# Optimization experiments

Measured on AMD Instinct MI355X. Metric: run time of the kernel, lower is better.

The kernel has to match this reference:

```python
import jax, jax.numpy as jnp
import numpy as np


def setup_inputs() -> dict:
    key = jax.random.key(0)
    k1, k2, k3, k4 = jax.random.split(key, 4)
    in_features, out_features = 4096, 11008
    n_tokens = 64
    x = jax.random.normal(k1, (n_tokens, in_features), dtype=jnp.float32)
    # int8-valued weights stored as int32 (values in [-128, 127] range subset)
    weight_int = jax.random.randint(k2, (out_features, in_features), 0, 127, dtype=jnp.int32)
    weight_scale = jnp.float32(0.01)
    weight_zero_point = 3  # scalar int zero point
    bias = jax.random.normal(k3, (out_features,), dtype=jnp.float32) * 0.02
    return {
        "x": x,
        "weight_int": weight_int,
        "weight_scale": weight_scale,
        "weight_zero_point": weight_zero_point,
        "bias": bias,
    }


def reference(x, weight_int, weight_scale, weight_zero_point, bias):
    # Dequantize: W = (W_int - zp) * scale, shape [out, in]
    w = (weight_int.astype(jnp.float32) - jnp.float32(weight_zero_point)) * weight_scale
    # F.linear: y = x @ W^T + b
    out = jnp.einsum("ti,oi->to", x, w)
    return out + bias
```

## Files before the change

### kernel.cpp

```cpp
#include <hip/hip_runtime.h>
#include <hip/hip_bf16.h>

typedef __attribute__((ext_vector_type(8))) short short8;
typedef __attribute__((ext_vector_type(4))) float f32x4;
typedef __attribute__((ext_vector_type(4))) int   int4v;

#define IN_F   4096
#define OUT_F  11008
#define KSPLIT 2
#define KHALF  (IN_F / KSPLIT)
#define BK     64
#define NIT    (KHALF / BK)
#define DEPTH  4

__device__ __forceinline__ short bf16_rne(float f) {
    unsigned u = __builtin_bit_cast(unsigned, f);
    u += 0x7FFFu + ((u >> 16) & 1u);
    return (short)(u >> 16);
}

__device__ __forceinline__ void gld16(const void* g, void* l) {
    __builtin_amdgcn_global_load_lds(
        (const __attribute__((address_space(1))) unsigned int*)g,
        (__attribute__((address_space(3))) unsigned int*)l,
        16, 0, 0);
}

__global__ __launch_bounds__(256)
void xcast(const float* __restrict__ x, unsigned short* __restrict__ xb) {
    const int i = (blockIdx.x * 256 + threadIdx.x) * 8;
    f32x4 a = *(const f32x4*)(x + i);
    f32x4 b = *(const f32x4*)(x + i + 4);
    short8 o;
#pragma unroll
    for (int j = 0; j < 4; ++j) { o[j] = bf16_rne(a[j]); o[j + 4] = bf16_rne(b[j]); }
    *(short8*)(xb + i) = o;
}

__global__ __launch_bounds__(256)
void binit(const float* __restrict__ bias, float* __restrict__ out) {
    const unsigned cid = blockIdx.x * 256 + threadIdx.x;
    const unsigned row = cid / (OUT_F / 8);
    const unsigned o   = (cid - row * (OUT_F / 8)) * 8;
    f32x4 b0 = *(const f32x4*)(bias + o);
    f32x4 b1 = *(const f32x4*)(bias + o + 4);
    float* dst = out + (size_t)row * OUT_F + o;
    *(f32x4*)dst = b0;
    *(f32x4*)(dst + 4) = b1;
}

#define STAGE(IT) do {                                                        \
    const int _s = (IT) & (DEPTH - 1);                                        \
    gld16(wsrc + (size_t)(IT) * BK,             (char*)wt[_s] + tid * 16);    \
    gld16(xsrc + (size_t)(IT) * BK,             (char*)xt[_s] + tid * 16);    \
    gld16(xsrc + (size_t)(IT) * BK + 32 * IN_F, (char*)xt[_s] + tid * 16 + 4096); \
} while (0)

#define KSTEP(S, KK) do {                                                     \
    const char* _wb = (const char*)wt[S] + l15 * 256;                         \
    const char* _ab = (const char*)xt[S] + (wv * 16 + l15) * 128;             \
    const int _cw = (KK) * 8 + lg * 2;                                        \
    const int _ca = (KK) * 4 + lg;                                            \
    int4v  _b0 = *(const int4v*)(_wb + (((_cw    ) ^ rswz) * 16));            \
    int4v  _b1 = *(const int4v*)(_wb + (((_cw + 1) ^ rswz) * 16));            \
    short8 _aw = *(const short8*)(_ab + ((_ca ^ rswz) * 16));                 \
    short8 _bw;                                                               \
    _Pragma("unroll")                                                         \
    for (int j = 0; j < 4; ++j) {                                             \
        float f0 = (float)(_b0[j] - zp);                                      \
        float f1 = (float)(_b1[j] - zp);                                      \
        _bw[j]     = (short)(__builtin_bit_cast(unsigned, f0) >> 16);         \
        _bw[j + 4] = (short)(__builtin_bit_cast(unsigned, f1) >> 16);         \
    }                                                                         \
    acc = __builtin_amdgcn_mfma_f32_16x16x32_bf16(_aw, _bw, acc, 0, 0, 0);    \
} while (0)

__global__ __launch_bounds__(256, 3)
void qlin5(const unsigned short* __restrict__ xb, const int* __restrict__ w,
           const float* __restrict__ scale_p, const int* __restrict__ zp_p,
           float* __restrict__ out)
{
    __shared__ __align__(16) int            wt[DEPTH][16 * BK];
    __shared__ __align__(16) unsigned short xt[DEPTH][64 * BK];

    const int tid  = threadIdx.x;
    const int lane = tid & 63;
    const int wv   = tid >> 6;
    const int l15  = lane & 15;
    const int lg   = lane >> 4;

    const int ob = blockIdx.x >> 1;
    const int kh = blockIdx.x & 1;
    const int o0 = ob * 16;
    const int kb = kh * KHALF;

    const int   zp    = zp_p[0];
    const float scale = scale_p[0];

    const int wr = tid >> 4;
    const int wc = (tid & 15) ^ (wr & 7);
    const int* wsrc = w + (size_t)(o0 + wr) * IN_F + kb + wc * 4;

    const int xr = tid >> 3;
    const int xc = (tid & 7) ^ (xr & 7);
    const unsigned short* xsrc = xb + (size_t)xr * IN_F + kb + xc * 8;

    const int rswz = l15 & 7;

    f32x4 acc = {0.f, 0.f, 0.f, 0.f};

    STAGE(0);
    STAGE(1);
    STAGE(2);

    for (int it = 0; it < NIT - 2; ++it) {
        asm volatile("s_waitcnt vmcnt(6)" ::: "memory");
        __builtin_amdgcn_s_barrier();
        if (it + 3 < NIT) STAGE(it + 3);
        const int s = it & (DEPTH - 1);
        KSTEP(s, 0);
        KSTEP(s, 1);
    }
    asm volatile("s_waitcnt vmcnt(3)" ::: "memory");
    __builtin_amdgcn_s_barrier();
    KSTEP((NIT - 2) & (DEPTH - 1), 0);
    KSTEP((NIT - 2) & (DEPTH - 1), 1);
    asm volatile("s_waitcnt vmcnt(0)" ::: "memory");
    __builtin_amdgcn_s_barrier();
    KSTEP((NIT - 1) & (DEPTH - 1), 0);
    KSTEP((NIT - 1) & (DEPTH - 1), 1);

    {
        const int o = o0 + l15;
#pragma unroll
        for (int r = 0; r < 4; ++r) {
            const int t = wv * 16 + lg * 4 + r;
            unsafeAtomicAdd(out + (size_t)t * OUT_F + o, scale * acc[r]);
        }
    }
}

extern "C" void kernel_launch(void* const* d_in, const int* in_sizes, int n_in,
                              void* d_out, int out_size, void* d_ws, size_t ws_size,
                              hipStream_t stream) {
    const float* x     = (const float*)d_in[0];
    const int*   w     = (const int*)d_in[1];
    const float* scale = (const float*)d_in[2];
    const int*   zp    = (const int*)d_in[3];
    const float* bias  = (const float*)d_in[4];
    float*       out   = (float*)d_out;
    unsigned short* xbf = (unsigned short*)d_ws;

    xcast<<<dim3(128), dim3(256), 0, stream>>>(x, xbf);
    binit<<<dim3(344), dim3(256), 0, stream>>>(bias, out);
    qlin5<<<dim3((OUT_F / 16) * KSPLIT), dim3(256), 0, stream>>>(xbf, w, scale, zp, out);
}
```

Before: 56.02 us.

## Widen output tile to 64 rows per block, dequantize once per wave, split K four ways

Each block now covers 64 output features instead of 16. Each wave dequantizes its own 16-row weight slice once per k-step and reuses it across four 16-token MFMAs, where before every wave re-dequantized the same shared weight tile. This cuts the redundant int-to-bf16 conversion and the LDS weight reads. The activation tile is now loaded once per 64 outputs instead of once per 16. To keep the grid large, K is split four ways with a 3-deep pipeline, which doubles the atomic-add traffic to the output and lowers occupancy to 2 blocks per CU because LDS per block grows.

```diff
diff --git a/kernel.cpp b/kernel.cpp
--- a/kernel.cpp
+++ b/kernel.cpp
@@ -7,11 +7,11 @@
 
 #define IN_F   4096
 #define OUT_F  11008
-#define KSPLIT 2
-#define KHALF  (IN_F / KSPLIT)
+#define KSPLIT 4
+#define KPART  (IN_F / KSPLIT)
 #define BK     64
-#define NIT    (KHALF / BK)
-#define DEPTH  4
+#define NIT    (KPART / BK)
+#define DEPTH  3
 
 __device__ __forceinline__ short bf16_rne(float f) {
     unsigned u = __builtin_bit_cast(unsigned, f);
@@ -24,6 +24,16 @@
         (const __attribute__((address_space(1))) unsigned int*)g,
         (__attribute__((address_space(3))) unsigned int*)l,
         16, 0, 0);
+}
+
+__device__ __forceinline__ short8 deq8(int4v q0, int4v q1, int zp) {
+    short8 r;
+#pragma unroll
+    for (int j = 0; j < 4; ++j) {
+        r[j]     = (short)(__builtin_bit_cast(unsigned, (float)(q0[j] - zp)) >> 16);
+        r[j + 4] = (short)(__builtin_bit_cast(unsigned, (float)(q1[j] - zp)) >> 16);
+    }
+    return r;
 }
 
 __global__ __launch_bounds__(256)
@@ -50,37 +60,51 @@
 }
 
 #define STAGE(IT) do {                                                        \
-    const int _s = (IT) & (DEPTH - 1);                                        \
-    gld16(wsrc + (size_t)(IT) * BK,             (char*)wt[_s] + tid * 16);    \
-    gld16(xsrc + (size_t)(IT) * BK,             (char*)xt[_s] + tid * 16);    \
-    gld16(xsrc + (size_t)(IT) * BK + 32 * IN_F, (char*)xt[_s] + tid * 16 + 4096); \
+    const int _s = (IT) % DEPTH;                                              \
+    const int* _wsi = wsrc + (size_t)(IT) * BK;                               \
+    gld16(_wsi,              (char*)wt[_s] + tid * 16);                       \
+    gld16(_wsi + 16 * IN_F,  (char*)wt[_s] + 4096  + tid * 16);               \
+    gld16(_wsi + 32 * IN_F,  (char*)wt[_s] + 8192  + tid * 16);               \
+    gld16(_wsi + 48 * IN_F,  (char*)wt[_s] + 12288 + tid * 16);               \
+    const unsigned short* _xsi = xsrc + (size_t)(IT) * BK;                    \
+    gld16(_xsi,            (char*)xt[_s] + tid * 16);                         \
+    gld16(_xsi + 32 * IN_F, (char*)xt[_s] + 4096 + tid * 16);                 \
 } while (0)
 
-#define KSTEP(S, KK) do {                                                     \
-    const char* _wb = (const char*)wt[S] + l15 * 256;                         \
-    const char* _ab = (const char*)xt[S] + (wv * 16 + l15) * 128;             \
-    const int _cw = (KK) * 8 + lg * 2;                                        \
-    const int _ca = (KK) * 4 + lg;                                            \
-    int4v  _b0 = *(const int4v*)(_wb + (((_cw    ) ^ rswz) * 16));            \
-    int4v  _b1 = *(const int4v*)(_wb + (((_cw + 1) ^ rswz) * 16));            \
-    short8 _aw = *(const short8*)(_ab + ((_ca ^ rswz) * 16));                 \
-    short8 _bw;                                                               \
-    _Pragma("unroll")                                                         \
-    for (int j = 0; j < 4; ++j) {                                             \
-        float f0 = (float)(_b0[j] - zp);                                      \
-        float f1 = (float)(_b1[j] - zp);                                      \
-        _bw[j]     = (short)(__builtin_bit_cast(unsigned, f0) >> 16);         \
-        _bw[j + 4] = (short)(__builtin_bit_cast(unsigned, f1) >> 16);         \
-    }                                                                         \
-    acc = __builtin_amdgcn_mfma_f32_16x16x32_bf16(_aw, _bw, acc, 0, 0, 0);    \
+#define COMPUTE(S) do {                                                       \
+    const char* _wb = (const char*)wt[S] + wrow_off;                          \
+    int4v _q00 = *(const int4v*)(_wb + cw00);                                 \
+    int4v _q01 = *(const int4v*)(_wb + cw01);                                 \
+    int4v _q10 = *(const int4v*)(_wb + cw10);                                 \
+    int4v _q11 = *(const int4v*)(_wb + cw11);                                 \
+    short8 _B0 = deq8(_q00, _q01, zp);                                        \
+    short8 _B1 = deq8(_q10, _q11, zp);                                        \
+    const char* _xb = (const char*)xt[S] + arow;                              \
+    short8 _a;                                                                \
+    _a = *(const short8*)(_xb +        ca0);                                  \
+    acc0 = __builtin_amdgcn_mfma_f32_16x16x32_bf16(_a, _B0, acc0, 0, 0, 0);   \
+    _a = *(const short8*)(_xb +        ca1);                                  \
+    acc0 = __builtin_amdgcn_mfma_f32_16x16x32_bf16(_a, _B1, acc0, 0, 0, 0);   \
+    _a = *(const short8*)(_xb + 2048 + ca0);                                  \
+    acc1 = __builtin_amdgcn_mfma_f32_16x16x32_bf16(_a, _B0, acc1, 0, 0, 0);   \
+    _a = *(const short8*)(_xb + 2048 + ca1);                                  \
+    acc1 = __builtin_amdgcn_mfma_f32_16x16x32_bf16(_a, _B1, acc1, 0, 0, 0);   \
+    _a = *(const short8*)(_xb + 4096 + ca0);                                  \
+    acc2 = __builtin_amdgcn_mfma_f32_16x16x32_bf16(_a, _B0, acc2, 0, 0, 0);   \
+    _a = *(const short8*)(_xb + 4096 + ca1);                                  \
+    acc2 = __builtin_amdgcn_mfma_f32_16x16x32_bf16(_a, _B1, acc2, 0, 0, 0);   \
+    _a = *(const short8*)(_xb + 6144 + ca0);                                  \
+    acc3 = __builtin_amdgcn_mfma_f32_16x16x32_bf16(_a, _B0, acc3, 0, 0, 0);   \
+    _a = *(const short8*)(_xb + 6144 + ca1);                                  \
+    acc3 = __builtin_amdgcn_mfma_f32_16x16x32_bf16(_a, _B1, acc3, 0, 0, 0);   \
 } while (0)
 
-__global__ __launch_bounds__(256, 3)
-void qlin5(const unsigned short* __restrict__ xb, const int* __restrict__ w,
+__global__ __launch_bounds__(256, 2)
+void qlin6(const unsigned short* __restrict__ xb, const int* __restrict__ w,
            const float* __restrict__ scale_p, const int* __restrict__ zp_p,
            float* __restrict__ out)
 {
-    __shared__ __align__(16) int            wt[DEPTH][16 * BK];
+    __shared__ __align__(16) int            wt[DEPTH][64 * BK];
     __shared__ __align__(16) unsigned short xt[DEPTH][64 * BK];
 
     const int tid  = threadIdx.x;
@@ -89,10 +113,10 @@
     const int l15  = lane & 15;
     const int lg   = lane >> 4;
 
-    const int ob = blockIdx.x >> 1;
-    const int kh = blockIdx.x & 1;
-    const int o0 = ob * 16;
-    const int kb = kh * KHALF;
+    const int ob = blockIdx.x >> 2;
+    const int kh = blockIdx.x & 3;
+    const int o0 = ob * 64;
+    const int kb = kh * KPART;
 
     const int   zp    = zp_p[0];
     const float scale = scale_p[0];
@@ -106,36 +130,44 @@
     const unsigned short* xsrc = xb + (size_t)xr * IN_F + kb + xc * 8;
 
     const int rswz = l15 & 7;
+    const int wrow_off = (wv * 16 + l15) * 256;
+    const int cw00 = ((lg * 2    ) ^ rswz) * 16;
+    const int cw01 = ((lg * 2 + 1) ^ rswz) * 16;
+    const int cw10 = ((8 + lg * 2    ) ^ rswz) * 16;
+    const int cw11 = ((8 + lg * 2 + 1) ^ rswz) * 16;
+    const int arow = l15 * 128;
+    const int ca0  = ((lg    ) ^ rswz) * 16;
+    const int ca1  = ((4 + lg) ^ rswz) * 16;
 
-    f32x4 acc = {0.f, 0.f, 0.f, 0.f};
+    f32x4 acc0 = {0.f, 0.f, 0.f, 0.f};
+    f32x4 acc1 = {0.f, 0.f, 0.f, 0.f};
+    f32x4 acc2 = {0.f, 0.f, 0.f, 0.f};
+    f32x4 acc3 = {0.f, 0.f, 0.f, 0.f};
 
     STAGE(0);
     STAGE(1);
-    STAGE(2);
 
-    for (int it = 0; it < NIT - 2; ++it) {
+#pragma unroll 3
+    for (int it = 0; it < NIT - 1; ++it) {
         asm volatile("s_waitcnt vmcnt(6)" ::: "memory");
         __builtin_amdgcn_s_barrier();
-        if (it + 3 < NIT) STAGE(it + 3);
-        const int s = it & (DEPTH - 1);
-        KSTEP(s, 0);
-        KSTEP(s, 1);
+        if (it + 2 < NIT) STAGE(it + 2);
+        COMPUTE(it % DEPTH);
     }
-    asm volatile("s_waitcnt vmcnt(3)" ::: "memory");
-    __builtin_amdgcn_s_barrier();
-    KSTEP((NIT - 2) & (DEPTH - 1), 0);
-    KSTEP((NIT - 2) & (DEPTH - 1), 1);
     asm volatile("s_waitcnt vmcnt(0)" ::: "memory");
     __builtin_amdgcn_s_barrier();
-    KSTEP((NIT - 1) & (DEPTH - 1), 0);
-    KSTEP((NIT - 1) & (DEPTH - 1), 1);
+    COMPUTE((NIT - 1) % DEPTH);
 
     {
-        const int o = o0 + l15;
+        const int o = o0 + wv * 16 + l15;
+        float* op = out + o;
 #pragma unroll
         for (int r = 0; r < 4; ++r) {
-            const int t = wv * 16 + lg * 4 + r;
-            unsafeAtomicAdd(out + (size_t)t * OUT_F + o, scale * acc[r]);
+            const int tr = lg * 4 + r;
+            unsafeAtomicAdd(op + (size_t)(tr     ) * OUT_F, scale * acc0[r]);
+            unsafeAtomicAdd(op + (size_t)(tr + 16) * OUT_F, scale * acc1[r]);
+            unsafeAtomicAdd(op + (size_t)(tr + 32) * OUT_F, scale * acc2[r]);
+            unsafeAtomicAdd(op + (size_t)(tr + 48) * OUT_F, scale * acc3[r]);
         }
     }
 }
@@ -153,5 +185,5 @@
 
     xcast<<<dim3(128), dim3(256), 0, stream>>>(x, xbf);
     binit<<<dim3(344), dim3(256), 0, stream>>>(bias, out);
-    qlin5<<<dim3((OUT_F / 16) * KSPLIT), dim3(256), 0, stream>>>(xbf, w, scale, zp, out);
+    qlin6<<<dim3((OUT_F / 64) * KSPLIT), dim3(256), 0, stream>>>(xbf, w, scale, zp, out);
 }
```

Result: faster. 47.97 us (-14.4%).
